# Optimization experiments

Measured on AMD Instinct MI355X. Metric: run time of the kernel, lower is better.

## Reference

```python
import jax, jax.numpy as jnp
import numpy as np

R = 8  # patch radius (init kwarg)


def setup_inputs() -> dict:
    key = jax.random.key(0)
    k1, k2, k3 = jax.random.split(key, 3)
    B, H, W, N = 8, 1024, 1024, 4096
    image1 = jax.random.normal(k1, (B, 1, H, W), dtype=jnp.float32)
    image2 = jax.random.normal(k2, (B, 1, H, W), dtype=jnp.float32)
    # (x1, y1, x2, y2) integer pixel coords in [0, H-1]
    matches = jax.random.randint(k3, (B, N, 4), 0, H, dtype=jnp.int32)
    return {"image1": image1, "image2": image2, "matches": matches}


def _normalize(p):
    # per-patch zero-mean / unit-std (unbiased std, matching torch.std)
    m = p.mean(axis=-1, keepdims=True)
    s = p.std(axis=-1, keepdims=True, ddof=1)
    return (p - m) / (s + 1e-4)


def reference(image1, image2, matches):
    r = R
    d = 2 * r + 1
    # offset grid, flattened row-major: lines[i,j]=i, columns[i,j]=j
    lines = jnp.repeat(jnp.arange(d, dtype=jnp.int32), d)   # [d^2]
    cols = jnp.tile(jnp.arange(d, dtype=jnp.int32), d)      # [d^2]
    # original M = [lines, columns, lines, columns]
    off = jnp.stack([lines, cols, lines, cols], axis=0)      # [4, d^2]
    idx = matches[..., None].astype(jnp.int32) + off          # [B, N, 4, d^2]

    def pad(im):  # [B,1,H,W] -> [B, H+2r, W+2r]
        return jnp.pad(im[:, 0], ((0, 0), (r, r), (r, r)))

    img1p, img2p = pad(image1), pad(image2)
    b = jnp.arange(matches.shape[0])[:, None, None]           # [B,1,1]
    # rows come from y-coord columns (1,3), cols from x-coord columns (0,2)
    p1 = img1p[b, idx[:, :, 1, :], idx[:, :, 0, :]]           # [B, N, d^2]
    p2 = img2p[b, idx[:, :, 3, :], idx[:, :, 2, :]]           # [B, N, d^2]
    return jnp.concatenate([_normalize(p1), _normalize(p2)], axis=-1)  # [B, N, 2*d^2]
```

## Files before the change

kernel.cpp:

```cpp
#include <hip/hip_runtime.h>
#include <hip/hip_bf16.h>


#define IMG_H 1024
#define IMG_W 1024
#define NMATCH 4096
#define DPATCH 17
#define NPATCH 289
#define RAD 8
#define HW (IMG_H * IMG_W)

__global__ __launch_bounds__(256) void prewarm_kernel(
    const float* __restrict__ img1,
    const float* __restrict__ img2)
{
    const int tid = blockIdx.x * blockDim.x + threadIdx.x;
    const int nthreads = gridDim.x * blockDim.x;
    const float4* __restrict__ a = (const float4*)img1;
    const float4* __restrict__ b = (const float4*)img2;
    const int n4 = (8 * HW) / 4;
    float s = 0.f;
    for (int i = tid; i < n4; i += nthreads) {
        float4 x = a[i];
        float4 y = b[i];
        s += x.x + x.y + x.z + x.w + y.x + y.y + y.z + y.w;
    }
    asm volatile("" :: "v"(s));
}

__global__ __launch_bounds__(256) void extract_patch_kernel(
    const float* __restrict__ img1,
    const float* __restrict__ img2,
    const int* __restrict__ matches,
    float* __restrict__ out)
{
    __shared__ float smem[4 * 4 * NPATCH];

    const int tid   = blockIdx.x * blockDim.x + threadIdx.x;
    const int wave  = tid >> 6;
    const int lane  = tid & 63;
    const int wslot = threadIdx.x >> 6;
    const int pair0 = wave << 1;

    const int g = lane / DPATCH;
    const int c = lane - g * DPATCH;
    const bool active = (g < 3);

    const int b = pair0 >> 12;
    const float* __restrict__ base1 = img1 + (size_t)b * HW;
    const float* __restrict__ base2 = img2 + (size_t)b * HW;

    int mx[4], my[4];
#pragma unroll
    for (int t = 0; t < 4; ++t) {
        const int pr = pair0 + (t >> 1);
        const int wh = t & 1;
        mx[t] = matches[pr * 4 + (wh ? 2 : 0)];
        my[t] = matches[pr * 4 + (wh ? 3 : 1)];
    }

    float v[4][6];
#pragma unroll
    for (int t = 0; t < 4; ++t) {
        const float* __restrict__ ib = (t & 1) ? base2 : base1;
        const int ix = mx[t] + c - RAD;
#pragma unroll
        for (int it = 0; it < 6; ++it) {
            const int r  = it * 3 + g;
            const int iy = my[t] + r - RAD;
            const bool ok = active && (r < DPATCH) &&
                            ((unsigned)ix < IMG_W) && ((unsigned)iy < IMG_H);
            const int off = ok ? (iy * IMG_W + ix) : 0;
            const float val = ib[off];
            v[t][it] = ok ? val : 0.f;
        }
    }

#pragma unroll
    for (int t = 0; t < 4; ++t) {
#pragma unroll
        for (int it = 0; it < 6; ++it) {
            const int r = it * 3 + g;
            if (active && r < DPATCH) {
                smem[(wslot * 4 + t) * NPATCH + r + DPATCH * c] = v[t][it];
            }
        }
    }

    float s[4], q[4];
#pragma unroll
    for (int t = 0; t < 4; ++t) {
        s[t] = 0.f; q[t] = 0.f;
#pragma unroll
        for (int it = 0; it < 6; ++it) {
            s[t] += v[t][it];
            q[t] += v[t][it] * v[t][it];
        }
    }
#pragma unroll
    for (int off = 32; off > 0; off >>= 1) {
#pragma unroll
        for (int t = 0; t < 4; ++t) {
            s[t] += __shfl_xor(s[t], off, 64);
            q[t] += __shfl_xor(q[t], off, 64);
        }
    }

    float* __restrict__ o0 = out + (size_t)pair0 * 578;
#pragma unroll
    for (int t = 0; t < 4; ++t) {
        const float mean = s[t] * (1.0f / 289.0f);
        float var = (q[t] - 289.0f * mean * mean) * (1.0f / 288.0f);
        var = fmaxf(var, 0.0f);
        const float inv = 1.0f / (sqrtf(var) + 1e-4f);
        float* __restrict__ o = o0 + t * NPATCH;
#pragma unroll
        for (int k = 0; k < 5; ++k) {
            const int j = lane + (k << 6);
            if (j < NPATCH) {
                const float z = (smem[(wslot * 4 + t) * NPATCH + j] - mean) * inv;
                __builtin_nontemporal_store(z, &o[j]);
            }
        }
    }
}

extern "C" void kernel_launch(void* const* d_in, const int* in_sizes, int n_in,
                              void* d_out, int out_size, void* d_ws, size_t ws_size,
                              hipStream_t stream) {
    const float* img1  = (const float*)d_in[0];
    const float* img2  = (const float*)d_in[1];
    const int* matches = (const int*)d_in[2];
    float* out         = (float*)d_out;

    hipLaunchKernelGGL(prewarm_kernel, dim3(2048), dim3(256), 0, stream,
                       img1, img2);

    hipLaunchKernelGGL(extract_patch_kernel, dim3(4096), dim3(256), 0, stream,
                       img1, img2, matches, out);
}
```

Measured before the change: 153.3 us.

## Bucket-sort patch tasks by image and row band; drop prewarm pass

Replaces the full-image prewarm read with a counting sort (histogram, scan, atomic scatter) that orders the 65536 patch tasks by batch, image and 16-row band of y. Each wave then gathers four spatially nearby patches, which is meant to improve cache locality for the scattered gathers. Output addresses are computed per task. This adds four small kernel launches and atomic contention, and without the prewarm the image data is no longer staged in cache beforehand.

```diff
diff --git a/kernel.cpp b/kernel.cpp
--- a/kernel.cpp
+++ b/kernel.cpp
@@ -9,29 +9,64 @@
 #define NPATCH 289
 #define RAD 8
 #define HW (IMG_H * IMG_W)
+#define NTASK 65536
+#define NBUCKET 1024
 
-__global__ __launch_bounds__(256) void prewarm_kernel(
-    const float* __restrict__ img1,
-    const float* __restrict__ img2)
-{
-    const int tid = blockIdx.x * blockDim.x + threadIdx.x;
-    const int nthreads = gridDim.x * blockDim.x;
-    const float4* __restrict__ a = (const float4*)img1;
-    const float4* __restrict__ b = (const float4*)img2;
-    const int n4 = (8 * HW) / 4;
-    float s = 0.f;
-    for (int i = tid; i < n4; i += nthreads) {
-        float4 x = a[i];
-        float4 y = b[i];
-        s += x.x + x.y + x.z + x.w + y.x + y.y + y.z + y.w;
+
+__device__ __forceinline__ int task_key(const int* matches, int t) {
+    const int pair  = t >> 1;
+    const int which = t & 1;
+    const int my = matches[pair * 4 + (which ? 3 : 1)];
+    return (((pair >> 12) << 1 | which) << 6) | ((my >> 4) & 63);
+}
+
+__global__ __launch_bounds__(256) void zero_hist_kernel(int* __restrict__ hist) {
+    const int i = threadIdx.x;
+#pragma unroll
+    for (int k = 0; k < NBUCKET / 256; ++k) hist[i + k * 256] = 0;
+}
+
+__global__ __launch_bounds__(256) void hist_kernel(
+    const int* __restrict__ matches, int* __restrict__ hist) {
+    const int t = blockIdx.x * blockDim.x + threadIdx.x;
+    atomicAdd(&hist[task_key(matches, t)], 1);
+}
+
+__global__ __launch_bounds__(64) void scan_kernel(int* __restrict__ hist) {
+    const int lane = threadIdx.x;
+    int local[16];
+    int s = 0;
+#pragma unroll
+    for (int i = 0; i < 16; ++i) {
+        local[i] = s;
+        s += hist[lane * 16 + i];
     }
-    asm volatile("" :: "v"(s));
+    int pre = s;
+#pragma unroll
+    for (int off = 1; off < 64; off <<= 1) {
+        int t = __shfl_up(pre, off, 64);
+        if (lane >= off) pre += t;
+    }
+    pre -= s;
+#pragma unroll
+    for (int i = 0; i < 16; ++i) {
+        hist[lane * 16 + i] = pre + local[i];
+    }
+}
+
+__global__ __launch_bounds__(256) void scatter_kernel(
+    const int* __restrict__ matches, int* __restrict__ hist,
+    int* __restrict__ tasks) {
+    const int t = blockIdx.x * blockDim.x + threadIdx.x;
+    const int pos = atomicAdd(&hist[task_key(matches, t)], 1);
+    tasks[pos] = t;
 }
 
 __global__ __launch_bounds__(256) void extract_patch_kernel(
     const float* __restrict__ img1,
     const float* __restrict__ img2,
     const int* __restrict__ matches,
+    const int* __restrict__ tasks,
     float* __restrict__ out)
 {
     __shared__ float smem[4 * 4 * NPATCH];
@@ -40,29 +75,29 @@
     const int wave  = tid >> 6;
     const int lane  = tid & 63;
     const int wslot = threadIdx.x >> 6;
-    const int pair0 = wave << 1;
 
     const int g = lane / DPATCH;
     const int c = lane - g * DPATCH;
     const bool active = (g < 3);
 
-    const int b = pair0 >> 12;
-    const float* __restrict__ base1 = img1 + (size_t)b * HW;
-    const float* __restrict__ base2 = img2 + (size_t)b * HW;
-
-    int mx[4], my[4];
+    int task[4], mx[4], my[4];
+    const float* ib[4];
+    float* op[4];
 #pragma unroll
     for (int t = 0; t < 4; ++t) {
-        const int pr = pair0 + (t >> 1);
-        const int wh = t & 1;
-        mx[t] = matches[pr * 4 + (wh ? 2 : 0)];
-        my[t] = matches[pr * 4 + (wh ? 3 : 1)];
+        task[t] = tasks[4 * wave + t];
+        const int pair  = task[t] >> 1;
+        const int which = task[t] & 1;
+        const int b = pair >> 12;
+        mx[t] = matches[pair * 4 + (which ? 2 : 0)];
+        my[t] = matches[pair * 4 + (which ? 3 : 1)];
+        ib[t] = (which ? img2 : img1) + (size_t)b * HW;
+        op[t] = out + (size_t)pair * 578 + which * NPATCH;
     }
 
     float v[4][6];
 #pragma unroll
     for (int t = 0; t < 4; ++t) {
-        const float* __restrict__ ib = (t & 1) ? base2 : base1;
         const int ix = mx[t] + c - RAD;
 #pragma unroll
         for (int it = 0; it < 6; ++it) {
@@ -71,7 +106,7 @@
             const bool ok = active && (r < DPATCH) &&
                             ((unsigned)ix < IMG_W) && ((unsigned)iy < IMG_H);
             const int off = ok ? (iy * IMG_W + ix) : 0;
-            const float val = ib[off];
+            const float val = ib[t][off];
             v[t][it] = ok ? val : 0.f;
         }
     }
@@ -106,20 +141,18 @@
         }
     }
 
-    float* __restrict__ o0 = out + (size_t)pair0 * 578;
 #pragma unroll
     for (int t = 0; t < 4; ++t) {
         const float mean = s[t] * (1.0f / 289.0f);
         float var = (q[t] - 289.0f * mean * mean) * (1.0f / 288.0f);
         var = fmaxf(var, 0.0f);
         const float inv = 1.0f / (sqrtf(var) + 1e-4f);
-        float* __restrict__ o = o0 + t * NPATCH;
 #pragma unroll
         for (int k = 0; k < 5; ++k) {
             const int j = lane + (k << 6);
             if (j < NPATCH) {
                 const float z = (smem[(wslot * 4 + t) * NPATCH + j] - mean) * inv;
-                __builtin_nontemporal_store(z, &o[j]);
+                __builtin_nontemporal_store(z, &op[t][j]);
             }
         }
     }
@@ -133,9 +166,16 @@
     const int* matches = (const int*)d_in[2];
     float* out         = (float*)d_out;
 
-    hipLaunchKernelGGL(prewarm_kernel, dim3(2048), dim3(256), 0, stream,
-                       img1, img2);
+    int* hist  = (int*)d_ws;
+    int* tasks = (int*)((char*)d_ws + 4096);
+
+    hipLaunchKernelGGL(zero_hist_kernel, dim3(1), dim3(256), 0, stream, hist);
+    hipLaunchKernelGGL(hist_kernel, dim3(NTASK / 256), dim3(256), 0, stream,
+                       matches, hist);
+    hipLaunchKernelGGL(scan_kernel, dim3(1), dim3(64), 0, stream, hist);
+    hipLaunchKernelGGL(scatter_kernel, dim3(NTASK / 256), dim3(256), 0, stream,
+                       matches, hist, tasks);
 
     hipLaunchKernelGGL(extract_patch_kernel, dim3(4096), dim3(256), 0, stream,
-                       img1, img2, matches, out);
+                       img1, img2, matches, tasks, out);
 }
```

Result: slower. 160.8 us (+4.9%).
